# Optimization experiments

Hardware: AMD Instinct MI355X
Metric: run time of the kernel (lower is better)

The kernel has to match this reference:

```python
import jax, jax.numpy as jnp
import numpy as np

DIM = 2048
NUM_HEADS = 16
NUM_KV_HEADS = 4
HEAD_DIM = DIM // NUM_HEADS  # 128
ROPE_BASE = 10000.0
TRAIN_SEQ_LEN = 1024
EPS = 1.1920929e-07  # torch.finfo(float32).eps, used by F.rms_norm default


def _rope_tables(seq_len, dtype=jnp.float32):
    rd = HEAD_DIM  # rope_dims defaults to full head_dim
    if seq_len > TRAIN_SEQ_LEN:
        s = seq_len / TRAIN_SEQ_LEN
        base = ROPE_BASE * s ** (rd / (rd - 2))
    else:
        base = ROPE_BASE
    inv_freq = 1.0 / base ** (jnp.arange(0, rd, 2, dtype=jnp.float32) / rd)
    t = jnp.arange(seq_len, dtype=jnp.float32)
    freqs = jnp.outer(t, inv_freq)  # [S, rd//2]
    cos = jnp.cos(freqs)[None, :, None, :].astype(dtype)  # [1,S,1,rd//2]
    sin = jnp.sin(freqs)[None, :, None, :].astype(dtype)
    return cos, sin


def _rms_norm(x):
    var = jnp.mean(jnp.square(x), axis=-1, keepdims=True)
    return x * jax.lax.rsqrt(var + EPS)


def _apply_rotary(x, cos, sin):
    h = x.shape[-1] // 2
    x1, x2 = x[..., :h], x[..., h:]
    return jnp.concatenate((x1 * cos + x2 * sin, -x1 * sin + x2 * cos), axis=-1)


def setup_inputs() -> dict:
    key = jax.random.key(0)
    ks = jax.random.split(key, 6)
    B, S = 2, 2048
    kv_dim = NUM_KV_HEADS * HEAD_DIM
    x = jax.random.normal(ks[0], (B, S, DIM), dtype=jnp.float32)
    Wq = jax.random.normal(ks[1], (DIM, DIM), dtype=jnp.float32) * 0.02
    Wk = jax.random.normal(ks[2], (kv_dim, DIM), dtype=jnp.float32) * 0.02
    Wv = jax.random.normal(ks[3], (kv_dim, DIM), dtype=jnp.float32) * 0.02
    Wo = jax.random.normal(ks[4], (DIM, DIM), dtype=jnp.float32) * 0.02
    q_gain = jnp.full((NUM_HEADS,), 1.0, dtype=jnp.float32)
    return {"x": x, "Wq": Wq, "Wk": Wk, "Wv": Wv, "Wo": Wo, "q_gain": q_gain}


def reference(x, Wq, Wk, Wv, Wo, q_gain):
    B, S, D = x.shape
    H, Hkv, Dh = NUM_HEADS, NUM_KV_HEADS, HEAD_DIM
    # QKV projections (CastedLinear, no bias)
    q = (x @ Wq.T).reshape(B, S, H, Dh)
    k = (x @ Wk.T).reshape(B, S, Hkv, Dh)
    v = (x @ Wv.T).reshape(B, S, Hkv, Dh)
    # RMSNorm over head_dim (no learned weight)
    q = _rms_norm(q)
    k = _rms_norm(k)
    # RoPE (full head_dim, NTK-scaled since S > train_seq_len)
    cos, sin = _rope_tables(S, q.dtype)
    q = _apply_rotary(q, cos, sin)
    k = _apply_rotary(k, cos, sin)
    # per-head gain on q
    q = q * q_gain.astype(q.dtype)[None, None, :, None]
    # GQA: repeat_interleave kv heads
    reps = H // Hkv
    k = jnp.repeat(k, reps, axis=2)  # [B,S,H,Dh]
    v = jnp.repeat(v, reps, axis=2)
    # causal attention
    scale = 1.0 / jnp.sqrt(jnp.asarray(Dh, dtype=q.dtype))
    scores = jnp.einsum('bqhd,bkhd->bhqk', q, k) * scale  # [B,H,S,S]
    causal = jnp.tril(jnp.ones((S, S), dtype=bool))
    scores = jnp.where(causal[None, None], scores, jnp.finfo(scores.dtype).min)
    attn = jax.nn.softmax(scores, axis=-1)
    y = jnp.einsum('bhqk,bkhd->bqhd', attn, v)  # [B,S,H,Dh]
    return y.reshape(B, S, D) @ Wo.T
```

## Files before the change

### kernel.cpp

```cpp
#include <hip/hip_runtime.h>

#define DIMSZ 2048
#define NHEAD 16
#define NKV 4
#define HD 128
#define QKVD 3072
#define SEQ 2048
#define NTOK 4096

typedef __attribute__((ext_vector_type(8))) short short8;
typedef __attribute__((ext_vector_type(4))) float f32x4;
typedef __attribute__((ext_vector_type(16))) float f32x16;
typedef unsigned short u16;

__device__ __forceinline__ u16 f2bf(float x) {
  union { float f; unsigned u; } v; v.f = x;
  unsigned r = v.u + 0x7fffu + ((v.u >> 16) & 1u);
  return (u16)(r >> 16);
}
__device__ __forceinline__ unsigned pack_bf2(float a, float b) {
  unsigned ua = __float_as_uint(a) + 0x8000u;
  unsigned ub = __float_as_uint(b) + 0x8000u;
  return __builtin_amdgcn_perm(ub, ua, 0x07060302);
}

__device__ __forceinline__ void gl_lds16(const void* g, void* l) {
  __builtin_amdgcn_global_load_lds(
      (const __attribute__((address_space(1))) void*)g,
      (__attribute__((address_space(3))) void*)l, 16, 0, 0);
}

template <int N> __device__ __forceinline__ void vmw() {
  asm volatile("s_waitcnt vmcnt(%0)" :: "n"(N) : "memory");
}
__device__ __forceinline__ void barsb() {
  __builtin_amdgcn_s_barrier();
  __builtin_amdgcn_sched_barrier(0);
}

__global__ __launch_bounds__(256)
void castAll(const float* __restrict__ x,  const float* __restrict__ Wq,
             const float* __restrict__ Wk, const float* __restrict__ Wv,
             const float* __restrict__ Wo, u16* __restrict__ xb,
             u16* __restrict__ Wqkvb, u16* __restrict__ Wob) {
  int i = blockIdx.x * 256 + threadIdx.x;
  int f = i * 4;
  const float* src; u16* dst; int off;
  if (f < 8388608)       { src = x;  dst = xb;    off = f; }
  else if (f < 12582912) { src = Wq; dst = Wqkvb; off = f - 8388608; }
  else if (f < 13631488) { src = Wk; dst = Wqkvb + 4194304; off = f - 12582912; }
  else if (f < 14680064) { src = Wv; dst = Wqkvb + 5242880; off = f - 13631488; }
  else                   { src = Wo; dst = Wob;   off = f - 14680064; }
  float4 v = *(const float4*)(src + off);
  ushort4 o;
  o.x = f2bf(v.x); o.y = f2bf(v.y); o.z = f2bf(v.z); o.w = f2bf(v.w);
  *(ushort4*)(dst + off) = o;
}

template <int NCT, bool F32OUT>
__global__ __launch_bounds__(512, 2)
void gemmX(const u16* __restrict__ A, const u16* __restrict__ W,
           void* __restrict__ Cv, int M, int N, int K) {
  __shared__ __align__(16) u16 As[2][256][64];
  __shared__ __align__(16) u16 Bs[2][NCT * 64][64];
  const int tid = threadIdx.x;
  const int l = tid & 63;
  const int w = tid >> 6;
  const int r = l & 15, q = l >> 4;
  const int wm = (w >> 2) * 128;
  const int wn = (w & 3) * (NCT * 16);

  const int nx  = N / (NCT * 64);
  const int cpx = gridDim.x >> 3;
  const int lid = (blockIdx.x & 7) * cpx + (blockIdx.x >> 3);
  const int m0 = (lid / nx) << 8;
  const int n0 = (lid % nx) * (NCT * 64);

  const int scol = ((l & 7) ^ (l >> 3)) << 3;
  const u16* Asrc = A + (long)(m0 + w * 8 + (l >> 3)) * K + scol;
  const u16* Bsrc = W + (long)(n0 + w * 8 + (l >> 3)) * K + scol;

  auto stA = [&](int d, int u, int kt) {
    gl_lds16(Asrc + (long)(u * 64) * K + kt * 64, &As[d][u * 64 + w * 8][0]);
  };
  auto stB = [&](int d, int u, int kt) {
    gl_lds16(Bsrc + (long)(u * 64) * K + kt * 64, &Bs[d][u * 64 + w * 8][0]);
  };
  auto lda = [&](int d, int rt, int ks) -> short8 {
    return *(const short8*)&As[d][wm + rt * 16 + r][(((ks << 2) | q) ^ (r & 7)) << 3];
  };
  auto ldb = [&](int d, int ct, int ks) -> short8 {
    return *(const short8*)&Bs[d][wn + ct * 16 + r][(((ks << 2) | q) ^ (r & 7)) << 3];
  };

  f32x4 acc[8][NCT] = {};
  short8 a[4][2];
  short8 bE[NCT][2];
  short8 bO[NCT][2];

#define QUAD(i_, AB, BR)                                                      \
  _Pragma("unroll") for (int ks_ = 0; ks_ < 2; ++ks_)                         \
  _Pragma("unroll") for (int c_ = 0; c_ < NCT; ++c_)                          \
    acc[(AB) + (i_)][c_] = __builtin_amdgcn_mfma_f32_16x16x32_bf16(           \
        a[i_][ks_], BR[c_][ks_], acc[(AB) + (i_)][c_], 0, 0, 0);

#pragma unroll
  for (int u = 0; u < NCT; ++u) stB(0, u, 0);
  stA(0, 0, 0); stA(0, 1, 0); stA(0, 2, 0); stA(0, 3, 0);
#pragma unroll
  for (int u = 0; u < NCT; ++u) stB(1, u, 1);
  stA(1, 0, 1); stA(1, 2, 1);
  vmw<NCT + 2>();
  barsb();
#pragma unroll
  for (int i = 0; i < 4; ++i) { a[i][0] = lda(0, i, 0); a[i][1] = lda(0, i, 1); }
#pragma unroll
  for (int c = 0; c < NCT; ++c) { bE[c][0] = ldb(0, c, 0); bE[c][1] = ldb(0, c, 1); }

  const int niter = K >> 7;
  for (int it = 0; it < niter; ++it) {
    const int kt1 = 2 * it + 1, kt2 = 2 * it + 2, kt3 = 2 * it + 3;
    const bool more = (it + 1 < niter);

    stA(1, 1, kt1); stA(1, 3, kt1);
    __builtin_amdgcn_s_setprio(1);
#pragma unroll
    for (int i_ = 0; i_ < 4; ++i_) {
      QUAD(i_, 0, bE);
      a[i_][0] = lda(0, 4 + i_, 0); a[i_][1] = lda(0, 4 + i_, 1);
    }
    __builtin_amdgcn_s_setprio(0);
    vmw<2>();
    barsb();

    if (more) {
#pragma unroll
      for (int u = 0; u < NCT; ++u) stB(0, u, kt2);
      stA(0, 0, kt2); stA(0, 2, kt2);
    }
    __builtin_amdgcn_s_setprio(1);
#pragma unroll
    for (int i_ = 0; i_ < 4; ++i_) {
      QUAD(i_, 4, bE);
      a[i_][0] = lda(1, i_, 0); a[i_][1] = lda(1, i_, 1);
      if (i_ == 0) {
#pragma unroll
        for (int c = 0; c < NCT; ++c) { bO[c][0] = ldb(1, c, 0); bO[c][1] = ldb(1, c, 1); }
      }
    }
    __builtin_amdgcn_s_setprio(0);
    if (more) vmw<NCT + 2>(); else vmw<0>();
    barsb();

    if (more) { stA(0, 1, kt2); stA(0, 3, kt2); }
    __builtin_amdgcn_s_setprio(1);
#pragma unroll
    for (int i_ = 0; i_ < 4; ++i_) {
      QUAD(i_, 0, bO);
      a[i_][0] = lda(1, 4 + i_, 0); a[i_][1] = lda(1, 4 + i_, 1);
    }
    __builtin_amdgcn_s_setprio(0);
    if (more) vmw<2>();
    barsb();

    if (more) {
#pragma unroll
      for (int u = 0; u < NCT; ++u) stB(1, u, kt3);
      stA(1, 0, kt3); stA(1, 2, kt3);
    }
    __builtin_amdgcn_s_setprio(1);
#pragma unroll
    for (int i_ = 0; i_ < 4; ++i_) {
      QUAD(i_, 4, bO);
      if (more) {
        a[i_][0] = lda(0, i_, 0); a[i_][1] = lda(0, i_, 1);
        if (i_ == 0) {
#pragma unroll
          for (int c = 0; c < NCT; ++c) { bE[c][0] = ldb(0, c, 0); bE[c][1] = ldb(0, c, 1); }
        }
      }
    }
    __builtin_amdgcn_s_setprio(0);
    if (more) vmw<NCT + 2>();
    barsb();
  }
#undef QUAD

#pragma unroll
  for (int i = 0; i < 8; ++i)
#pragma unroll
    for (int j = 0; j < NCT; ++j) {
      int row = m0 + wm + i * 16 + q * 4;
      int col = n0 + wn + j * 16 + r;
#pragma unroll
      for (int t = 0; t < 4; ++t) {
        if (F32OUT)
          ((float*)Cv)[(long)(row + t) * N + col] = acc[i][j][t];
        else
          ((u16*)Cv)[(long)(row + t) * N + col] = f2bf(acc[i][j][t]);
      }
    }
}

__global__ __launch_bounds__(256)
void prep(u16* __restrict__ qkv, const float* __restrict__ gain, float qsc,
          u16* __restrict__ vt) {
  if (blockIdx.x < 20480) {
    int gid  = blockIdx.x * 4 + (threadIdx.x >> 6);
    int lane = threadIdx.x & 63;
    int token = gid / 20;
    int idx   = gid % 20;
    int s     = token & (SEQ - 1);
    bool isq  = idx < 16;
    int off   = isq ? idx * HD : 2048 + (idx - 16) * HD;
    float psc = isq ? qsc * gain[idx & 15] : 1.0f;
    u16* p = qkv + (long)token * QKVD + off;
    union { unsigned u; float f; } c1, c2;
    c1.u = ((unsigned)p[lane]) << 16;
    c2.u = ((unsigned)p[lane + 64]) << 16;
    float x1 = c1.f, x2 = c2.f;
    float ss = x1 * x1 + x2 * x2;
#pragma unroll
    for (int d = 1; d < 64; d <<= 1) ss += __shfl_xor(ss, d);
    float rn = rsqrtf(ss * (1.0f / 128.0f) + 1.1920929e-07f) * psc;
    float lb = log2f(10000.0f) + 128.0f / 126.0f;
    float inv_freq = exp2f(-(float)lane * (lb * (1.0f / 64.0f)));
    float ang = (float)s * inv_freq;
    float sn, cs;
    sincosf(ang, &sn, &cs);
    p[lane]      = f2bf((x1 * cs + x2 * sn) * rn);
    p[lane + 64] = f2bf((-x1 * sn + x2 * cs) * rn);
  } else {
    __shared__ u16 T[128 * 72];
    int bid = blockIdx.x - 20480;
    const int k0 = (bid & 31) * 64, hkv = (bid >> 5) & 3, b = bid >> 7;
    const u16* vb = qkv + 2560;
    const int t = threadIdx.x;
    const int key = t & 63, dh0 = (t >> 6) * 32;
#pragma unroll
    for (int c = 0; c < 4; c++) {
      uint4 vv = *(const uint4*)&vb[(long)(b * SEQ + k0 + key) * QKVD + hkv * HD + dh0 + c * 8];
      u16 tmp[8];
      *(uint4*)tmp = vv;
#pragma unroll
      for (int e = 0; e < 8; e++) T[(dh0 + c * 8 + e) * 72 + key] = tmp[e];
    }
    __syncthreads();
    const int dh = t >> 1, half = t & 1;
#pragma unroll
    for (int c = 0; c < 4; c++) {
      uint4 ov = *(const uint4*)&T[dh * 72 + half * 32 + c * 8];
      *(uint4*)&vt[((long)(b * NKV + hkv) * HD + dh) * SEQ + k0 + half * 32 + c * 8] = ov;
    }
  }
}

__global__ __launch_bounds__(256, 2)
void fattn(const u16* __restrict__ qb, const u16* __restrict__ kb,
           const u16* __restrict__ vtg, u16* __restrict__ yb) {
  __shared__ u16 Ks[64 * 128];
  __shared__ u16 Vt[128 * 64];
  const int tid = threadIdx.x;
  const int l   = tid & 63;
  const int w   = tid >> 6;
  const int lh  = l >> 5;
  const int l31 = l & 31;
  const int bq  = blockIdx.x >> 5;
  const int qt  = (blockIdx.x & 256) ? (bq - 8) : (15 - bq);
  const int hb  = blockIdx.x & 31;
  const int h   = hb >> 1;
  const int b   = hb & 1;
  const int q0  = qt * 128;
  const int hkv = h >> 2;
  const int qrow = q0 + w * 32 + l31;

  int koff[4], voff[4];
  u16 *kdst[4], *vdst[4];
#pragma unroll
  for (int c = 0; c < 4; c++) {
    int gr = w * 16 + c * 4 + (l >> 4);
    int s  = l & 15;
    int kj = s ^ (gr & 15);
    koff[c] = gr * QKVD + hkv * HD + kj * 8;
    kdst[c] = Ks + (w * 16 + c * 4) * 128;
    int dh = w * 32 + c * 8 + (l >> 3);
    int vs = l & 7;
    int vj = vs ^ (dh & 7);
    voff[c] = dh * SEQ + vj * 8;
    vdst[c] = Vt + (w * 32 + c * 8) * 64;
  }
  const u16* vbase = vtg + (long)(b * NKV + hkv) * HD * SEQ;

  short8 qf[8];
  {
    const u16* qp = qb + (long)(b * SEQ + qrow) * QKVD + h * HD + lh * 8;
#pragma unroll
    for (int ks = 0; ks < 8; ks++)
      qf[ks] = *(const short8*)(qp + ks * 16);
  }

  f32x16 oacc[4] = {};
  float l_i = 0.f;

  auto kfr = [&](int kt, int ks) -> short8 {
    int row = kt * 32 + l31;
    int p = (ks * 2 + lh) ^ (row & 15);
    return *(const short8*)&Ks[row * 128 + p * 8];
  };
  auto vfr = [&](int dt, int kq) -> short8 {
    int row = dt * 32 + l31;
    int p = (kq * 2 + lh) ^ (row & 7);
    return *(const short8*)&Vt[row * 64 + p * 8];
  };

  const int kend = q0 + 64;
  for (int k0 = 0; k0 <= kend; k0 += 64) {
    __syncthreads();
    const u16* kb_t = kb + (long)(b * SEQ + k0) * QKVD;
    const u16* vb_t = vbase + k0;
#pragma unroll
    for (int c = 0; c < 4; c++) {
      gl_lds16(kb_t + koff[c], kdst[c]);
      gl_lds16(vb_t + voff[c], vdst[c]);
    }
    __syncthreads();

    const bool diag = (k0 >= q0);

#pragma unroll
    for (int kt = 0; kt < 2; ++kt) {
      f32x16 st;
#pragma unroll
      for (int g = 0; g < 16; ++g) st[g] = 0.f;
#pragma unroll
      for (int ks = 0; ks < 8; ++ks)
        st = __builtin_amdgcn_mfma_f32_32x32x16_bf16(kfr(kt, ks), qf[ks], st, 0, 0, 0);

      if (diag) {
#pragma unroll
        for (int g = 0; g < 16; ++g) {
          int key = k0 + kt * 32 + (g & 3) + 8 * (g >> 2) + 4 * lh;
          if (key > qrow) st[g] = -3e38f;
        }
      }

#pragma unroll
      for (int g = 0; g < 16; ++g) {
        float e = exp2f(st[g]);
        st[g] = e;
        l_i += e;
      }

      unsigned c8[8];
#pragma unroll
      for (int m = 0; m < 8; ++m) c8[m] = pack_bf2(st[2 * m], st[2 * m + 1]);
      asm("v_permlane32_swap_b32 %0, %1" : "+v"(c8[0]), "+v"(c8[2]));
      asm("v_permlane32_swap_b32 %0, %1" : "+v"(c8[1]), "+v"(c8[3]));
      asm("v_permlane32_swap_b32 %0, %1" : "+v"(c8[4]), "+v"(c8[6]));
      asm("v_permlane32_swap_b32 %0, %1" : "+v"(c8[5]), "+v"(c8[7]));
      union { unsigned u[4]; short8 s; } pa0, pa1;
      pa0.u[0] = c8[0]; pa0.u[1] = c8[1]; pa0.u[2] = c8[2]; pa0.u[3] = c8[3];
      pa1.u[0] = c8[4]; pa1.u[1] = c8[5]; pa1.u[2] = c8[6]; pa1.u[3] = c8[7];

#pragma unroll
      for (int dt = 0; dt < 4; ++dt) {
        oacc[dt] = __builtin_amdgcn_mfma_f32_32x32x16_bf16(pa0.s, vfr(dt, kt * 2 + 0), oacc[dt], 0, 0, 0);
        oacc[dt] = __builtin_amdgcn_mfma_f32_32x32x16_bf16(pa1.s, vfr(dt, kt * 2 + 1), oacc[dt], 0, 0, 0);
      }
    }
  }

  l_i += __shfl_xor(l_i, 32);
  float linv = 1.0f / l_i;
#pragma unroll
  for (int g = 0; g < 16; ++g) {
    int qrl = (g & 3) + 8 * (g >> 2) + 4 * lh;
    float lg = __shfl(linv, qrl);
    long rowoff = (long)(b * SEQ + q0 + w * 32 + qrl) * DIMSZ + h * HD + l31;
#pragma unroll
    for (int dt = 0; dt < 4; ++dt)
      yb[rowoff + dt * 32] = f2bf(oacc[dt][g] * lg);
  }
}

extern "C" void kernel_launch(void* const* d_in, const int* in_sizes, int n_in,
                              void* d_out, int out_size, void* d_ws, size_t ws_size,
                              hipStream_t stream) {
  const float* x  = (const float*)d_in[0];
  const float* Wq = (const float*)d_in[1];
  const float* Wk = (const float*)d_in[2];
  const float* Wv = (const float*)d_in[3];
  const float* Wo = (const float*)d_in[4];
  const float* qg = (const float*)d_in[5];
  float* out = (float*)d_out;

  const long MB = 1024 * 1024;
  char* ws = (char*)d_ws;
  u16* xb    = (u16*)(ws + 0 * MB);
  u16* ybuf  = (u16*)(ws + 0 * MB);
  u16* Wqkvb = (u16*)(ws + 16 * MB);
  u16* Wob   = (u16*)(ws + 28 * MB);
  u16* qkv   = (u16*)(ws + 36 * MB);
  u16* vtg   = (u16*)(ws + 60 * MB);

  castAll<<<18432, 256, 0, stream>>>(x, Wq, Wk, Wv, Wo, xb, Wqkvb, Wob);

  gemmX<3, false><<<256, 512, 0, stream>>>(xb, Wqkvb, qkv, NTOK, QKVD, DIMSZ);

  const float qsc = 0.08838834764831845f * 1.44269504088896f;
  prep<<<20736, 256, 0, stream>>>(qkv, qg, qsc, vtg);

  fattn<<<512, 256, 0, stream>>>(qkv, qkv + 2048, vtg, ybuf);

  gemmX<2, true><<<256, 512, 0, stream>>>(ybuf, Wob, out, NTOK, DIMSZ, DIMSZ);
}
```

Before: 303.7 us.

## Double-buffer K/V tiles in LDS to overlap loads with attention compute

Doubles the shared-memory K and V buffers and restructures the key loop into a two-stage ping-pong: the next 64-key tile is issued via global-to-LDS loads before computing on the current one. The goal is to hide global load latency behind MFMA work and cut one barrier per tile. The cost is doubled LDS per block (64KB), which may limit occupancy below the two blocks per CU requested by the launch bounds.

```diff
diff --git a/kernel.cpp b/kernel.cpp
--- a/kernel.cpp
+++ b/kernel.cpp
@@ -258,8 +258,8 @@
 __global__ __launch_bounds__(256, 2)
 void fattn(const u16* __restrict__ qb, const u16* __restrict__ kb,
            const u16* __restrict__ vtg, u16* __restrict__ yb) {
-  __shared__ u16 Ks[64 * 128];
-  __shared__ u16 Vt[128 * 64];
+  __shared__ u16 Ks[2 * 64 * 128];
+  __shared__ u16 Vt[2 * 128 * 64];
   const int tid = threadIdx.x;
   const int l   = tid & 63;
   const int w   = tid >> 6;
@@ -302,44 +302,35 @@
   f32x16 oacc[4] = {};
   float l_i = 0.f;
 
-  auto kfr = [&](int kt, int ks) -> short8 {
-    int row = kt * 32 + l31;
-    int p = (ks * 2 + lh) ^ (row & 15);
-    return *(const short8*)&Ks[row * 128 + p * 8];
-  };
-  auto vfr = [&](int dt, int kq) -> short8 {
-    int row = dt * 32 + l31;
-    int p = (kq * 2 + lh) ^ (row & 7);
-    return *(const short8*)&Vt[row * 64 + p * 8];
-  };
-
-  const int kend = q0 + 64;
-  for (int k0 = 0; k0 <= kend; k0 += 64) {
-    __syncthreads();
-    const u16* kb_t = kb + (long)(b * SEQ + k0) * QKVD;
-    const u16* vb_t = vbase + k0;
+  auto stage = [&](int k0n, int bo) {
+    const u16* kb_n = kb + (long)(b * SEQ + k0n) * QKVD;
+    const u16* vb_n = vbase + k0n;
 #pragma unroll
     for (int c = 0; c < 4; c++) {
-      gl_lds16(kb_t + koff[c], kdst[c]);
-      gl_lds16(vb_t + voff[c], vdst[c]);
-    }
-    __syncthreads();
-
-    const bool diag = (k0 >= q0);
-
+      gl_lds16(kb_n + koff[c], kdst[c] + bo);
+      gl_lds16(vb_n + voff[c], vdst[c] + bo);
+    }
+  };
+
+  auto compute = [&](int k0c, const u16* ksb, const u16* vtb) {
+    const bool diag = (k0c >= q0);
 #pragma unroll
     for (int kt = 0; kt < 2; ++kt) {
       f32x16 st;
 #pragma unroll
       for (int g = 0; g < 16; ++g) st[g] = 0.f;
 #pragma unroll
-      for (int ks = 0; ks < 8; ++ks)
-        st = __builtin_amdgcn_mfma_f32_32x32x16_bf16(kfr(kt, ks), qf[ks], st, 0, 0, 0);
+      for (int ks = 0; ks < 8; ++ks) {
+        int row = kt * 32 + l31;
+        int p = (ks * 2 + lh) ^ (row & 15);
+        short8 kf = *(const short8*)&ksb[row * 128 + p * 8];
+        st = __builtin_amdgcn_mfma_f32_32x32x16_bf16(kf, qf[ks], st, 0, 0, 0);
+      }
 
       if (diag) {
 #pragma unroll
         for (int g = 0; g < 16; ++g) {
-          int key = k0 + kt * 32 + (g & 3) + 8 * (g >> 2) + 4 * lh;
+          int key = k0c + kt * 32 + (g & 3) + 8 * (g >> 2) + 4 * lh;
           if (key > qrow) st[g] = -3e38f;
         }
       }
@@ -364,10 +355,28 @@
 
 #pragma unroll
       for (int dt = 0; dt < 4; ++dt) {
-        oacc[dt] = __builtin_amdgcn_mfma_f32_32x32x16_bf16(pa0.s, vfr(dt, kt * 2 + 0), oacc[dt], 0, 0, 0);
-        oacc[dt] = __builtin_amdgcn_mfma_f32_32x32x16_bf16(pa1.s, vfr(dt, kt * 2 + 1), oacc[dt], 0, 0, 0);
-      }
-    }
+        int row = dt * 32 + l31;
+        int p0 = ((kt * 2 + 0) * 2 + lh) ^ (row & 7);
+        int p1 = ((kt * 2 + 1) * 2 + lh) ^ (row & 7);
+        short8 vf0 = *(const short8*)&vtb[row * 64 + p0 * 8];
+        short8 vf1 = *(const short8*)&vtb[row * 64 + p1 * 8];
+        oacc[dt] = __builtin_amdgcn_mfma_f32_32x32x16_bf16(pa0.s, vf0, oacc[dt], 0, 0, 0);
+        oacc[dt] = __builtin_amdgcn_mfma_f32_32x32x16_bf16(pa1.s, vf1, oacc[dt], 0, 0, 0);
+      }
+    }
+  };
+
+  const int kend = q0 + 64;
+  stage(0, 0);
+  for (int k0 = 0; k0 < kend; k0 += 128) {
+    __syncthreads();
+    __builtin_amdgcn_sched_barrier(0);
+    stage(k0 + 64, 8192);
+    compute(k0, Ks, Vt);
+    __syncthreads();
+    __builtin_amdgcn_sched_barrier(0);
+    if (k0 + 128 <= kend) stage(k0 + 128, 0);
+    compute(k0 + 64, Ks + 8192, Vt + 8192);
   }
 
   l_i += __shfl_xor(l_i, 32);
```

Result: faster. 292.6 us (-3.6%).
